# Kernel tuning notes

Measured on AMD Instinct MI355X. Metric: run time of the kernel, lower is better.

The kernel has to match this reference:

```python
import jax, jax.numpy as jnp
import numpy as np

DIM = 512

def setup_inputs() -> dict:
    key = jax.random.key(0)
    kx, kq, kk, kv = jax.random.split(key, 4)
    x = jax.random.normal(kx, (8, 2048, DIM), dtype=jnp.float32)
    # Dense kernels are [in_dim, out_dim], no bias
    Wq = jax.random.normal(kq, (DIM, DIM), dtype=jnp.float32) * (DIM ** -0.5)
    Wk = jax.random.normal(kk, (DIM, DIM), dtype=jnp.float32) * (DIM ** -0.5)
    Wv = jax.random.normal(kv, (DIM, DIM), dtype=jnp.float32) * (DIM ** -0.5)
    return {"x": x, "Wq": Wq, "Wk": Wk, "Wv": Wv}

def reference(x, Wq, Wk, Wv):
    # x: [b, s, d]
    q = jnp.einsum('bsd,de->bse', x, Wq)
    k = jnp.einsum('bsd,de->bse', x, Wk)
    v = jnp.einsum('bsd,de->bse', x, Wv)
    scale = jnp.sqrt(jnp.asarray(DIM, dtype=x.dtype))
    attn = jnp.einsum('bqe,bke->bqk', q, k) / scale  # [b, s, s]
    attn = jax.nn.softmax(attn, axis=-1)
    return jnp.einsum('bqk,bke->bqe', attn, v)  # [b, s, d]
```

## Files before the change

### kernel.cpp

```cpp
#include <hip/hip_runtime.h>
#include <stdint.h>

typedef unsigned short u16;
typedef unsigned int u32;
typedef float floatx4 __attribute__((ext_vector_type(4)));
typedef __bf16 bf16x8 __attribute__((ext_vector_type(8)));
typedef __attribute__((address_space(1))) const u32 gu32;
typedef __attribute__((address_space(3))) u32 lu32;

#define SEQ 2048
#define DIM 512
#define NBATCH 8
#define TOTS (NBATCH * SEQ)

#if defined(__has_builtin)
#if __has_builtin(__builtin_amdgcn_cvt_pk_bf16_f32)
#define HAVE_PK_BF16 1
#endif
#endif
#ifndef HAVE_PK_BF16
#define HAVE_PK_BF16 0
#endif

__device__ __forceinline__ u16 f2bf(float f) {
#if HAVE_PK_BF16
  auto p = __builtin_amdgcn_cvt_pk_bf16_f32(f, f);
  union { decltype(p) v; u16 u[2]; } cv; cv.v = p;
  return cv.u[0];
#else
  u32 u = __float_as_uint(f);
  u += 0x7fffu + ((u >> 16) & 1u);
  return (u16)(u >> 16);
#endif
}

__device__ __forceinline__ void stage_tile64(const u16* __restrict__ g, int ld, int k0, u16* lds) {
  const int t = threadIdx.x;
  const int wave = t >> 6, lane = t & 63;
  const int rsub = lane >> 3;
  const int lg = (lane & 7) ^ rsub;
#pragma unroll
  for (int q = 0; q < 4; ++q) {
    const int chunk = wave * 4 + q;
    const int row = chunk * 8 + rsub;
    const u16* gp = g + (size_t)row * ld + k0 + lg * 8;
    u16* lp = lds + chunk * 512 + lane * 8;
    __builtin_amdgcn_global_load_lds((gu32*)gp, (lu32*)lp, 16, 0, 0);
  }
}

__device__ __forceinline__ void gemm_core(const u16* A, const u16* BT, int lda, int ldb, int kdim,
                                          u16* As, u16* Bs, floatx4 acc[4][4]) {
  const int t = threadIdx.x;
  const int wave = t >> 6, lane = t & 63;
  const int wr = (wave >> 1) * 64, wc = (wave & 1) * 64;
  const int l15 = lane & 15, quad = lane >> 4;
  const int swz = l15 & 7;
  stage_tile64(A, lda, 0, As);
  stage_tile64(BT, ldb, 0, Bs);
  __syncthreads();
  int cur = 0;
  for (int k0 = 0; k0 < kdim; k0 += 64) {
    const int lastiter = (k0 + 64 >= kdim);
    if (!lastiter) {
      stage_tile64(A, lda, k0 + 64, As + ((cur ^ 1) * (128 * 64)));
      stage_tile64(BT, ldb, k0 + 64, Bs + ((cur ^ 1) * (128 * 64)));
    }
    const u16* Ac = As + cur * (128 * 64);
    const u16* Bc = Bs + cur * (128 * 64);
#pragma unroll
    for (int ks = 0; ks < 2; ++ks) {
      const int pg = ((ks << 2) + quad) ^ swz;
      bf16x8 af[4], bfr[4];
#pragma unroll
      for (int i = 0; i < 4; ++i) {
        af[i]  = *(const bf16x8*)(Ac + (wr + i * 16 + l15) * 64 + pg * 8);
        bfr[i] = *(const bf16x8*)(Bc + (wc + i * 16 + l15) * 64 + pg * 8);
      }
#pragma unroll
      for (int mi = 0; mi < 4; ++mi)
#pragma unroll
        for (int ni = 0; ni < 4; ++ni)
          acc[mi][ni] = __builtin_amdgcn_mfma_f32_16x16x32_bf16(af[mi], bfr[ni], acc[mi][ni], 0, 0, 0);
    }
    if (!lastiter) __syncthreads();
    cur ^= 1;
  }
}

__device__ __forceinline__ void zero_acc(floatx4 acc[4][4]) {
#pragma unroll
  for (int i = 0; i < 4; ++i)
#pragma unroll
    for (int j = 0; j < 4; ++j)
      acc[i][j] = (floatx4){0.f, 0.f, 0.f, 0.f};
}

__global__ __launch_bounds__(256) void k_prep(const float* __restrict__ x,
                                              const float* __restrict__ Wq, const float* __restrict__ Wk,
                                              const float* __restrict__ Wv,
                                              u16* __restrict__ xb, u16* __restrict__ wt) {
  __shared__ float tile[64][65];
  const int t = threadIdx.x;
  if (blockIdx.x < 4096) {
    size_t i = ((size_t)blockIdx.x * 256 + t) * 8;
    float4 a = *(const float4*)(x + i);
    float4 b = *(const float4*)(x + i + 4);
    u16 o[8] = {f2bf(a.x), f2bf(a.y), f2bf(a.z), f2bf(a.w),
                f2bf(b.x), f2bf(b.y), f2bf(b.z), f2bf(b.w)};
    *(uint4*)(xb + i) = *(const uint4*)o;
    return;
  }
  const int r = blockIdx.x - 4096;
  const int sec = r >> 6, rem = r & 63;
  const int kb = (rem & 7) * 64, nb0 = (rem >> 3) * 64;
  const float* W = (sec == 0) ? Wq : (sec == 1) ? Wk : Wv;
#pragma unroll
  for (int i = 0; i < 4; ++i) {
    int kr = i * 16 + (t >> 4), nc = (t & 15) * 4;
    float4 v = *(const float4*)&W[(size_t)(kb + kr) * 512 + nb0 + nc];
    tile[kr][nc] = v.x; tile[kr][nc + 1] = v.y; tile[kr][nc + 2] = v.z; tile[kr][nc + 3] = v.w;
  }
  __syncthreads();
#pragma unroll
  for (int i = 0; i < 4; ++i) {
    int nr = i * 16 + (t >> 4), kc = (t & 15) * 4;
    u16 o[4] = {f2bf(tile[kc][nr]), f2bf(tile[kc + 1][nr]), f2bf(tile[kc + 2][nr]), f2bf(tile[kc + 3][nr])};
    *(uint2*)&wt[(size_t)(sec * 512 + nb0 + nr) * 512 + kb + kc] = *(const uint2*)o;
  }
}

__global__ __launch_bounds__(256, 4) void k_qkv(const u16* __restrict__ xb, const u16* __restrict__ wt,
                                                u16* __restrict__ qo, u16* __restrict__ ko) {
  __shared__ __align__(16) u16 As[2 * 128 * 64];
  __shared__ __align__(16) u16 Bs[2 * 128 * 64];
  const int m0 = blockIdx.x * 128, n0 = blockIdx.y * 128;
  floatx4 acc[4][4];
  zero_acc(acc);
  gemm_core(xb + (size_t)m0 * DIM, wt + (size_t)n0 * DIM, DIM, DIM, DIM, As, Bs, acc);
  const int t = threadIdx.x, wave = t >> 6, lane = t & 63;
  const int wr = (wave >> 1) * 64, wc = (wave & 1) * 64;
  const int l15 = lane & 15, quad = lane >> 4;
  const int sec = n0 >> 9;
  u16* __restrict__ C = sec ? ko : qo;
  const float scl = sec ? 1.0f : 0.04419417382415922f;
#pragma unroll
  for (int mi = 0; mi < 4; ++mi)
#pragma unroll
    for (int ni = 0; ni < 4; ++ni)
#pragma unroll
      for (int r = 0; r < 4; ++r) {
        int m = m0 + wr + mi * 16 + quad * 4 + r;
        int nc = (n0 + wc + ni * 16 + l15) & 511;
        C[(size_t)m * DIM + nc] = f2bf(acc[mi][ni][r] * scl);
      }
}

__global__ __launch_bounds__(256, 4) void k_vt(const u16* __restrict__ xb, const u16* __restrict__ wt,
                                               u16* __restrict__ vt) {
  __shared__ __align__(16) u16 As[2 * 128 * 64];
  __shared__ __align__(16) u16 Bs[2 * 128 * 64];
  const int m0 = blockIdx.x * 128;
  const int n0 = blockIdx.y * 128;
  floatx4 acc[4][4];
  zero_acc(acc);
  gemm_core(wt + (size_t)(2 * DIM + m0) * DIM, xb + (size_t)n0 * DIM, DIM, DIM, DIM, As, Bs, acc);
  const int t = threadIdx.x, wave = t >> 6, lane = t & 63;
  const int wr = (wave >> 1) * 64, wc = (wave & 1) * 64;
  const int l15 = lane & 15, quad = lane >> 4;
#pragma unroll
  for (int mi = 0; mi < 4; ++mi)
#pragma unroll
    for (int ni = 0; ni < 4; ++ni)
#pragma unroll
      for (int r = 0; r < 4; ++r) {
        int m = m0 + wr + mi * 16 + quad * 4 + r;
        int n = n0 + wc + ni * 16 + l15;
        vt[(size_t)m * TOTS + n] = f2bf(acc[mi][ni][r]);
      }
}

__global__ __launch_bounds__(256, 4) void k_scores(const u16* __restrict__ q, const u16* __restrict__ kk,
                                                   u16* __restrict__ sc, float* __restrict__ rowsum,
                                                   int b0) {
  __shared__ __align__(16) u16 As[2 * 128 * 64];
  __shared__ __align__(16) u16 Bs[2 * 128 * 64];
  const int bz = blockIdx.z, bb = b0 + bz;
  const int xcd = blockIdx.x & 7, j = blockIdx.x >> 3;
  const int m0 = (j & 15) * 128, n0 = (xcd * 2 + (j >> 4)) * 128;
  floatx4 acc[4][4];
  zero_acc(acc);
  gemm_core(q + (size_t)bb * SEQ * DIM + (size_t)m0 * DIM,
            kk + (size_t)bb * SEQ * DIM + (size_t)n0 * DIM, DIM, DIM, DIM, As, Bs, acc);
  u16* C = sc + (size_t)bz * SEQ * SEQ;
  float* rsb = rowsum + (size_t)bb * SEQ;
  const int t = threadIdx.x, wave = t >> 6, lane = t & 63;
  const int wr = (wave >> 1) * 64, wc = (wave & 1) * 64;
  const int l15 = lane & 15, quad = lane >> 4;
#pragma unroll
  for (int mi = 0; mi < 4; ++mi)
#pragma unroll
    for (int r = 0; r < 4; ++r) {
      int m = m0 + wr + mi * 16 + quad * 4 + r;
      float p = 0.f;
      float ev[4];
#pragma unroll
      for (int ni = 0; ni < 4; ++ni) {
        ev[ni] = __expf(acc[mi][ni][r]);
        p += ev[ni];
      }
#pragma unroll
      for (int ni = 0; ni < 4; ++ni) {
        int n = n0 + wc + ni * 16 + l15;
        C[(size_t)m * SEQ + n] = f2bf(ev[ni]);
      }
      p += __shfl_xor(p, 1); p += __shfl_xor(p, 2);
      p += __shfl_xor(p, 4); p += __shfl_xor(p, 8);
      if (l15 == 0) atomicAdd(&rsb[m], p);
    }
}

__global__ __launch_bounds__(256, 4) void k_pv(const u16* __restrict__ sc, const u16* __restrict__ vt,
                                               const float* __restrict__ rowsum,
                                               float* __restrict__ out, int b0) {
  __shared__ __align__(16) u16 As[2 * 128 * 64];
  __shared__ __align__(16) u16 Bs[2 * 128 * 64];
  const int bz = blockIdx.z, bb = b0 + bz;
  const int xcd = blockIdx.x & 7, j = blockIdx.x >> 3;
  const int m0 = (xcd * 2 + (j & 1)) * 128, n0 = (j >> 1) * 128;
  floatx4 acc[4][4];
  zero_acc(acc);
  gemm_core(sc + (size_t)bz * SEQ * SEQ + (size_t)m0 * SEQ,
            vt + (size_t)n0 * TOTS + (size_t)bb * SEQ, SEQ, TOTS, SEQ, As, Bs, acc);
  float* C = out + (size_t)bb * SEQ * DIM;
  const float* rsb = rowsum + (size_t)bb * SEQ;
  const int t = threadIdx.x, wave = t >> 6, lane = t & 63;
  const int wr = (wave >> 1) * 64, wc = (wave & 1) * 64;
  const int l15 = lane & 15, quad = lane >> 4;
#pragma unroll
  for (int mi = 0; mi < 4; ++mi)
#pragma unroll
    for (int r = 0; r < 4; ++r) {
      int m = m0 + wr + mi * 16 + quad * 4 + r;
      float inv = 1.0f / rsb[m];
#pragma unroll
      for (int ni = 0; ni < 4; ++ni) {
        int n = n0 + wc + ni * 16 + l15;
        C[(size_t)m * DIM + n] = acc[mi][ni][r] * inv;
      }
    }
}

extern "C" void kernel_launch(void* const* d_in, const int* in_sizes, int n_in,
                              void* d_out, int out_size, void* d_ws, size_t ws_size,
                              hipStream_t stream) {
  const float* x  = (const float*)d_in[0];
  const float* Wq = (const float*)d_in[1];
  const float* Wk = (const float*)d_in[2];
  const float* Wv = (const float*)d_in[3];
  float* out = (float*)d_out;
  char* ws = (char*)d_ws;

  u16* xb   = (u16*)(ws + 0);
  u16* wt   = (u16*)(ws + 16777216);
  u16* qo   = (u16*)(ws + 18350080);
  u16* ko   = (u16*)(ws + 35127296);
  u16* vt   = (u16*)(ws + 51904512);
  float* rs = (float*)(ws + 68681728);
  u16* sc   = (u16*)(ws + 68747264);
  const size_t base_need = 68747264;
  const size_t per_b = (size_t)SEQ * SEQ * 2;
  size_t avail = (ws_size > base_need) ? (ws_size - base_need) : 0;
  int nb = (int)(avail / per_b);
  if (nb < 1) nb = 1;
  if (nb > NBATCH) nb = NBATCH;

  hipMemsetAsync(rs, 0, (size_t)NBATCH * SEQ * sizeof(float), stream);
  k_prep<<<dim3(4288), dim3(256), 0, stream>>>(x, Wq, Wk, Wv, xb, wt);
  k_qkv<<<dim3(128, 8), dim3(256), 0, stream>>>(xb, wt, qo, ko);
  k_vt<<<dim3(4, 128), dim3(256), 0, stream>>>(xb, wt, vt);
  for (int b0 = 0; b0 < NBATCH; b0 += nb) {
    int nbr = (NBATCH - b0 < nb) ? (NBATCH - b0) : nb;
    k_scores<<<dim3(256, 1, nbr), dim3(256), 0, stream>>>(qo, ko, sc, rs, b0);
    k_pv<<<dim3(64, 1, nbr), dim3(256), 0, stream>>>(sc, vt, rs, out, b0);
  }
}
```

Before: 229.7 us.

## Fuse scores and PV into a single flash-style attention kernel

Replaces the separate scores kernel (which wrote bf16 exp-scores to a workspace buffer and used atomic row sums) and the PV kernel with one fused kernel. Each block keeps a 64-row Q tile in registers, streams K tiles through double-buffered LDS, exponentiates into an LDS P tile, and multiplies by V read straight from global memory. Row sums are reduced on chip, so the score matrix round-trip through HBM, the memset and the atomics go away. The trade-off is a grid of only 256 blocks at occupancy 1 with heavy register pressure, plus uncached V loads from global memory.

```diff
diff --git a/kernel.cpp b/kernel.cpp
--- a/kernel.cpp
+++ b/kernel.cpp
@@ -32,6 +32,10 @@
   u += 0x7fffu + ((u >> 16) & 1u);
   return (u16)(u >> 16);
 #endif
+}
+
+__device__ __forceinline__ u32 pkbf2(float lo, float hi) {
+  return ((u32)f2bf(hi) << 16) | (u32)f2bf(lo);
 }
 
 __device__ __forceinline__ void stage_tile64(const u16* __restrict__ g, int ld, int k0, u16* lds) {
@@ -180,73 +184,135 @@
       }
 }
 
-__global__ __launch_bounds__(256, 4) void k_scores(const u16* __restrict__ q, const u16* __restrict__ kk,
-                                                   u16* __restrict__ sc, float* __restrict__ rowsum,
-                                                   int b0) {
-  __shared__ __align__(16) u16 As[2 * 128 * 64];
-  __shared__ __align__(16) u16 Bs[2 * 128 * 64];
-  const int bz = blockIdx.z, bb = b0 + bz;
-  const int xcd = blockIdx.x & 7, j = blockIdx.x >> 3;
-  const int m0 = (j & 15) * 128, n0 = (xcd * 2 + (j >> 4)) * 128;
-  floatx4 acc[4][4];
-  zero_acc(acc);
-  gemm_core(q + (size_t)bb * SEQ * DIM + (size_t)m0 * DIM,
-            kk + (size_t)bb * SEQ * DIM + (size_t)n0 * DIM, DIM, DIM, DIM, As, Bs, acc);
-  u16* C = sc + (size_t)bz * SEQ * SEQ;
-  float* rsb = rowsum + (size_t)bb * SEQ;
-  const int t = threadIdx.x, wave = t >> 6, lane = t & 63;
-  const int wr = (wave >> 1) * 64, wc = (wave & 1) * 64;
+__global__ __launch_bounds__(256, 1) void k_attn(const u16* __restrict__ qo, const u16* __restrict__ ko,
+                                                 const u16* __restrict__ vt, float* __restrict__ out) {
+  __shared__ __align__(16) u16 Ks[2 * 2 * 128 * 64];
+  __shared__ __align__(16) u16 Ps[64 * 128];
+  __shared__ float rsbuf[4][32];
+  const int t = threadIdx.x, w = t >> 6, lane = t & 63;
   const int l15 = lane & 15, quad = lane >> 4;
+  const int swz = l15 & 7;
+  const int bb = blockIdx.x & 7, qt = blockIdx.x >> 3;
+  const int q0g = bb * SEQ + qt * 64;
+  const int h_q = w & 1, h_kv = w >> 1;
+
+  bf16x8 qf[16][2];
+#pragma unroll
+  for (int kc = 0; kc < 16; ++kc)
+#pragma unroll
+    for (int ni = 0; ni < 2; ++ni) {
+      int qrow = q0g + h_q * 32 + ni * 16 + l15;
+      qf[kc][ni] = *(const bf16x8*)(qo + (size_t)qrow * DIM + kc * 32 + quad * 8);
+    }
+
+  floatx4 Oacc[4][8];
+#pragma unroll
+  for (int i = 0; i < 4; ++i)
+#pragma unroll
+    for (int j = 0; j < 8; ++j)
+      Oacc[i][j] = (floatx4){0.f, 0.f, 0.f, 0.f};
+  float rs0 = 0.f, rs1 = 0.f;
+
+  const u16* Kbase = ko + (size_t)(bb * SEQ) * DIM;
+  const u16* Vbase = vt + (size_t)(bb * SEQ);
+
+  stage_tile64(Kbase, DIM, 0, Ks);
+  stage_tile64(Kbase, DIM, 64, Ks + 8192);
+  __syncthreads();
+  int cur = 0;
+
+  for (int kt = 0; kt < 16; ++kt) {
+    floatx4 Sacc[4][2];
+#pragma unroll
+    for (int i = 0; i < 4; ++i)
+#pragma unroll
+      for (int j = 0; j < 2; ++j)
+        Sacc[i][j] = (floatx4){0.f, 0.f, 0.f, 0.f};
+
+    for (int c = 0; c < 4; ++c) {
+      if (!(kt == 15 && c == 3)) {
+        int nc = c + 1;
+        int nkt = kt + (nc >> 2); nc &= 3;
+        const u16* kb = Kbase + (size_t)(nkt * 128) * DIM;
+        u16* dst = Ks + (cur ^ 1) * 16384;
+        stage_tile64(kb, DIM, nc * 128, dst);
+        stage_tile64(kb, DIM, nc * 128 + 64, dst + 8192);
+      }
+      const u16* Kc = Ks + cur * 16384;
+#pragma unroll
+      for (int ks = 0; ks < 4; ++ks) {
+        const int pg = ((ks & 1) * 4 + quad) ^ swz;
+        const u16* Ku = Kc + (ks >> 1) * 8192;
+        bf16x8 af[4];
+#pragma unroll
+        for (int mi = 0; mi < 4; ++mi)
+          af[mi] = *(const bf16x8*)(Ku + (h_kv * 64 + mi * 16 + l15) * 64 + pg * 8);
+#pragma unroll
+        for (int mi = 0; mi < 4; ++mi)
+#pragma unroll
+          for (int ni = 0; ni < 2; ++ni)
+            Sacc[mi][ni] = __builtin_amdgcn_mfma_f32_16x16x32_bf16(af[mi], qf[c * 4 + ks][ni],
+                                                                   Sacc[mi][ni], 0, 0, 0);
+      }
+      __syncthreads();
+      cur ^= 1;
+    }
+
+#pragma unroll
+    for (int mi = 0; mi < 4; ++mi)
+#pragma unroll
+      for (int ni = 0; ni < 2; ++ni) {
+        float e0 = __expf(Sacc[mi][ni][0]);
+        float e1 = __expf(Sacc[mi][ni][1]);
+        float e2 = __expf(Sacc[mi][ni][2]);
+        float e3 = __expf(Sacc[mi][ni][3]);
+        float s = (e0 + e1) + (e2 + e3);
+        if (ni == 0) rs0 += s; else rs1 += s;
+        uint2 pk;
+        pk.x = pkbf2(e0, e1);
+        pk.y = pkbf2(e2, e3);
+        int qrow = h_q * 32 + ni * 16 + l15;
+        int kv = h_kv * 64 + mi * 16 + quad * 4;
+        int g = (kv >> 3) ^ (qrow & 7);
+        *(uint2*)((char*)Ps + qrow * 256 + g * 16 + (quad & 1) * 8) = pk;
+      }
+    __syncthreads();
+
+#pragma unroll
+    for (int ksl = 0; ksl < 4; ++ksl) {
+      bf16x8 pa[4], bv[8];
+#pragma unroll
+      for (int mi = 0; mi < 4; ++mi) {
+        int qrow = mi * 16 + l15;
+        int g = ((ksl * 4 + quad) ^ (qrow & 7));
+        pa[mi] = *(const bf16x8*)((const char*)Ps + qrow * 256 + g * 16);
+      }
+#pragma unroll
+      for (int ne = 0; ne < 8; ++ne) {
+        int e = w * 128 + ne * 16 + l15;
+        bv[ne] = *(const bf16x8*)(Vbase + (size_t)e * TOTS + kt * 128 + ksl * 32 + quad * 8);
+      }
+#pragma unroll
+      for (int mi = 0; mi < 4; ++mi)
+#pragma unroll
+        for (int ne = 0; ne < 8; ++ne)
+          Oacc[mi][ne] = __builtin_amdgcn_mfma_f32_16x16x32_bf16(pa[mi], bv[ne], Oacc[mi][ne], 0, 0, 0);
+    }
+  }
+
+  rs0 += __shfl_xor(rs0, 16); rs0 += __shfl_xor(rs0, 32);
+  rs1 += __shfl_xor(rs1, 16); rs1 += __shfl_xor(rs1, 32);
+  if (lane < 16) { rsbuf[w][l15] = rs0; rsbuf[w][16 + l15] = rs1; }
+  __syncthreads();
 #pragma unroll
   for (int mi = 0; mi < 4; ++mi)
 #pragma unroll
     for (int r = 0; r < 4; ++r) {
-      int m = m0 + wr + mi * 16 + quad * 4 + r;
-      float p = 0.f;
-      float ev[4];
-#pragma unroll
-      for (int ni = 0; ni < 4; ++ni) {
-        ev[ni] = __expf(acc[mi][ni][r]);
-        p += ev[ni];
-      }
-#pragma unroll
-      for (int ni = 0; ni < 4; ++ni) {
-        int n = n0 + wc + ni * 16 + l15;
-        C[(size_t)m * SEQ + n] = f2bf(ev[ni]);
-      }
-      p += __shfl_xor(p, 1); p += __shfl_xor(p, 2);
-      p += __shfl_xor(p, 4); p += __shfl_xor(p, 8);
-      if (l15 == 0) atomicAdd(&rsb[m], p);
-    }
-}
-
-__global__ __launch_bounds__(256, 4) void k_pv(const u16* __restrict__ sc, const u16* __restrict__ vt,
-                                               const float* __restrict__ rowsum,
-                                               float* __restrict__ out, int b0) {
-  __shared__ __align__(16) u16 As[2 * 128 * 64];
-  __shared__ __align__(16) u16 Bs[2 * 128 * 64];
-  const int bz = blockIdx.z, bb = b0 + bz;
-  const int xcd = blockIdx.x & 7, j = blockIdx.x >> 3;
-  const int m0 = (xcd * 2 + (j & 1)) * 128, n0 = (j >> 1) * 128;
-  floatx4 acc[4][4];
-  zero_acc(acc);
-  gemm_core(sc + (size_t)bz * SEQ * SEQ + (size_t)m0 * SEQ,
-            vt + (size_t)n0 * TOTS + (size_t)bb * SEQ, SEQ, TOTS, SEQ, As, Bs, acc);
-  float* C = out + (size_t)bb * SEQ * DIM;
-  const float* rsb = rowsum + (size_t)bb * SEQ;
-  const int t = threadIdx.x, wave = t >> 6, lane = t & 63;
-  const int wr = (wave >> 1) * 64, wc = (wave & 1) * 64;
-  const int l15 = lane & 15, quad = lane >> 4;
-#pragma unroll
-  for (int mi = 0; mi < 4; ++mi)
-#pragma unroll
-    for (int r = 0; r < 4; ++r) {
-      int m = m0 + wr + mi * 16 + quad * 4 + r;
-      float inv = 1.0f / rsb[m];
-#pragma unroll
-      for (int ni = 0; ni < 4; ++ni) {
-        int n = n0 + wc + ni * 16 + l15;
-        C[(size_t)m * DIM + n] = acc[mi][ni][r] * inv;
+      int ql = mi * 16 + quad * 4 + r;
+      float inv = 1.f / (rsbuf[ql >> 5][ql & 31] + rsbuf[(ql >> 5) + 2][ql & 31]);
+#pragma unroll
+      for (int ne = 0; ne < 8; ++ne) {
+        out[(size_t)(q0g + ql) * DIM + w * 128 + ne * 16 + l15] = Oacc[mi][ne][r] * inv;
       }
     }
 }
@@ -266,22 +332,9 @@
   u16* qo   = (u16*)(ws + 18350080);
   u16* ko   = (u16*)(ws + 35127296);
   u16* vt   = (u16*)(ws + 51904512);
-  float* rs = (float*)(ws + 68681728);
-  u16* sc   = (u16*)(ws + 68747264);
-  const size_t base_need = 68747264;
-  const size_t per_b = (size_t)SEQ * SEQ * 2;
-  size_t avail = (ws_size > base_need) ? (ws_size - base_need) : 0;
-  int nb = (int)(avail / per_b);
-  if (nb < 1) nb = 1;
-  if (nb > NBATCH) nb = NBATCH;
-
-  hipMemsetAsync(rs, 0, (size_t)NBATCH * SEQ * sizeof(float), stream);
+
   k_prep<<<dim3(4288), dim3(256), 0, stream>>>(x, Wq, Wk, Wv, xb, wt);
   k_qkv<<<dim3(128, 8), dim3(256), 0, stream>>>(xb, wt, qo, ko);
   k_vt<<<dim3(4, 128), dim3(256), 0, stream>>>(xb, wt, vt);
-  for (int b0 = 0; b0 < NBATCH; b0 += nb) {
-    int nbr = (NBATCH - b0 < nb) ? (NBATCH - b0) : nb;
-    k_scores<<<dim3(256, 1, nbr), dim3(256), 0, stream>>>(qo, ko, sc, rs, b0);
-    k_pv<<<dim3(64, 1, nbr), dim3(256), 0, stream>>>(sc, vt, rs, out, b0);
-  }
-}
+  k_attn<<<dim3(256), dim3(256), 0, stream>>>(qo, ko, vt, out);
+}
```

Measured after the change: 259.1 us. +12.8%, slower.
